# Optimization experiments

Hardware: AMD Instinct MI355X
Metric: run time of the kernel (lower is better)

The kernel has to match this reference:

```python
import jax, jax.numpy as jnp
import numpy as np

N = 20000      # nodes (B in the original code)
T = 8          # timesteps
D_IN = 256     # in_dim (must equal hid_dim due to conv_h_n reuse in original)
D_HID = 256
D_OUT = 64
E = 320000     # edges


def setup_inputs() -> dict:
    key = jax.random.key(0)
    ks = jax.random.split(key, 18)
    s = 0.05
    w = lambda k, shape: jax.random.normal(k, shape, jnp.float32) * s
    return {
        "x": jax.random.normal(ks[0], (N, T, D_IN), jnp.float32),
        "edge_index": jax.random.randint(ks[1], (2, E), 0, N),
        "W_xr": w(ks[2], (D_IN, D_HID)),  "b_xr": w(ks[3], (D_HID,)),
        "W_hr": w(ks[4], (D_HID, D_HID)), "b_hr": w(ks[5], (D_HID,)),
        "W_xz": w(ks[6], (D_IN, D_HID)),  "b_xz": w(ks[7], (D_HID,)),
        "W_hz": w(ks[8], (D_HID, D_HID)), "b_hz": w(ks[9], (D_HID,)),
        "W_hn": w(ks[10], (D_HID, D_HID)), "b_hn": w(ks[11], (D_HID,)),
        "W_fc": w(ks[12], (D_HID, D_OUT)), "b_fc": w(ks[13], (D_OUT,)),
    }


def reference(x, edge_index, W_xr, b_xr, W_hr, b_hr, W_xz, b_xz, W_hz, b_hz,
              W_hn, b_hn, W_fc, b_fc):
    n_nodes = x.shape[0]
    src, dst = edge_index[0], edge_index[1]

    # GCN symmetric normalization with self-loops (PyG GCNConv default):
    # deg[i] = 1 + #incoming edges; norm_e = d^-1/2[src]*d^-1/2[dst]
    deg = jax.ops.segment_sum(jnp.ones(src.shape[0], x.dtype), dst,
                              num_segments=n_nodes) + jnp.asarray(1.0, x.dtype)
    dis = jax.lax.rsqrt(deg)
    enorm = dis[src] * dis[dst]      # [E]
    snorm = dis * dis                # self-loop coefficient 1/deg, [N]

    def gcn(v, W, b):
        vw = v @ W                                              # [N, D]
        agg = jax.ops.segment_sum(vw[src] * enorm[:, None], dst,
                                  num_segments=n_nodes)
        return agg + vw * snorm[:, None] + b

    def step(h, x_t):
        r = jax.nn.sigmoid(gcn(x_t, W_xr, b_xr) + gcn(h, W_hr, b_hr))
        z = jax.nn.sigmoid(gcn(x_t, W_xz, b_xz) + gcn(h, W_hz, b_hz))
        # faithful to original: conv_h_n is applied to BOTH x and h
        n = jnp.tanh(gcn(x_t, W_hn, b_hn) + r * gcn(h, W_hn, b_hn))
        h_new = (1.0 - z) * h + z * n
        return h_new, None

    h0 = jnp.zeros((n_nodes, W_hr.shape[0]), x.dtype)
    h, _ = jax.lax.scan(step, h0, jnp.transpose(x, (1, 0, 2)))  # scan over T
    return h @ W_fc + b_fc
```

## Files before the change

### kernel.cpp

```cpp
#include <hip/hip_runtime.h>
#include <hip/hip_bf16.h>
#include <math.h>

#define N_NODES 20000
#define T_STEPS 8
#define DDIM    256
#define DOUT    64
#define NE      320000
#define G4      1024
#define XSTR    2048

typedef unsigned short u16;
typedef __attribute__((ext_vector_type(8))) short  short8;
typedef __attribute__((ext_vector_type(4))) float  f32x4;

__device__ __forceinline__ float bf2f(u16 u) {
    union { unsigned int i; float f; } v; v.i = ((unsigned int)u) << 16; return v.f;
}
__device__ __forceinline__ u16 f2bf(float f) {
    union { float f; unsigned int i; } v; v.f = f;
    unsigned int r = v.i + 0x7fff + ((v.i >> 16) & 1);
    return (u16)(r >> 16);
}

__global__ void k_count(const int* __restrict__ dst, int* __restrict__ cnt) {
    int e = blockIdx.x * blockDim.x + threadIdx.x;
    if (e < NE) atomicAdd(&cnt[dst[e]], 1);
}

__global__ void k_degnorm(const int* __restrict__ cnt, float* __restrict__ dis,
                          float* __restrict__ snorm) {
    int n = blockIdx.x * blockDim.x + threadIdx.x;
    if (n < N_NODES) {
        float deg = (float)(cnt[n] + 1);
        dis[n]   = rsqrtf(deg);
        snorm[n] = 1.0f / deg;
    }
}

__global__ void k_scan(const int* __restrict__ cnt, int* __restrict__ rowptr) {
    __shared__ int sums[256];
    const int CH = (N_NODES + 255) / 256;
    int t = threadIdx.x;
    int beg = t * CH;
    int end = beg + CH; if (end > N_NODES) end = N_NODES;
    int s = 0;
    for (int i = beg; i < end; i++) s += cnt[i];
    sums[t] = s;
    __syncthreads();
    if (t == 0) {
        int run = 0;
        for (int i = 0; i < 256; i++) { int v = sums[i]; sums[i] = run; run += v; }
    }
    __syncthreads();
    if (beg < N_NODES) {
        int run = sums[t];
        for (int i = beg; i < end; i++) { rowptr[i] = run; run += cnt[i]; }
        if (end == N_NODES) rowptr[N_NODES] = run;
    }
}

__global__ void k_fill(const int* __restrict__ src, const int* __restrict__ dst,
                       const int* __restrict__ rowptr, int* __restrict__ cursor,
                       const float* __restrict__ dis, int* __restrict__ csr_src,
                       float* __restrict__ csr_norm) {
    int e = blockIdx.x * blockDim.x + threadIdx.x;
    if (e < NE) {
        int d = dst[e], s = src[e];
        int pos = atomicAdd(&cursor[d], 1);
        int i = rowptr[d] + pos;
        if (i < NE) {
            csr_src[i]  = s;
            csr_norm[i] = dis[s] * dis[d];
        }
    }
}

__global__ void k_pack4T(const float* __restrict__ Wa, const float* __restrict__ Wb,
                         const float* __restrict__ Wc, const float* __restrict__ Wd,
                         u16* __restrict__ out) {
    int i = blockIdx.x * blockDim.x + threadIdx.x;
    if (i < G4 * DDIM) {
        int c = i >> 8, k = i & 255;
        const float* W = (c < 256) ? Wa : (c < 512) ? Wb : (c < 768) ? Wc : Wd;
        int cc = c & 255;
        out[i] = f2bf(W[k * DDIM + cc]);
    }
}
__global__ void k_packb4(const float* __restrict__ bxr, const float* __restrict__ bhr,
                         const float* __restrict__ bxz, const float* __restrict__ bhz,
                         const float* __restrict__ bhn, float* __restrict__ bout) {
    int c = blockIdx.x * blockDim.x + threadIdx.x;
    if (c < G4) {
        float v;
        if (c < 256)      v = bxr[c] + bhr[c];
        else if (c < 512) v = bxz[c - 256] + bhz[c - 256];
        else              v = bhn[c & 255];
        bout[c] = v;
    }
}

__global__ __launch_bounds__(256) void k_x2bf_all(const float* __restrict__ x,
                                                  u16* __restrict__ out) {
    int i = blockIdx.x * blockDim.x + threadIdx.x;
    if (i >= N_NODES * 512) return;
    size_t o = (size_t)i << 2;
    float4 v = *(const float4*)(x + o);
    ushort4 u; u.x = f2bf(v.x); u.y = f2bf(v.y); u.z = f2bf(v.z); u.w = f2bf(v.w);
    *(ushort4*)(out + o) = u;
}

__global__ __launch_bounds__(256) void k_agg_x(const u16* __restrict__ xall,
                      const int* __restrict__ rowptr, const int* __restrict__ csr_src,
                      const float* __restrict__ csr_norm, const float* __restrict__ snorm,
                      u16* __restrict__ xaall) {
    int n = blockIdx.x * 4 + (threadIdx.x >> 6);
    if (n >= N_NODES) return;
    int lane = threadIdx.x & 63;
    int c4 = lane << 2;
    float sn = snorm[n];
    float acc[8][4];
    const u16* selfp = xall + (size_t)n * XSTR + c4;
#pragma unroll
    for (int t = 0; t < 8; t++) {
        ushort4 v = *(const ushort4*)(selfp + t * DDIM);
        acc[t][0] = bf2f(v.x) * sn; acc[t][1] = bf2f(v.y) * sn;
        acc[t][2] = bf2f(v.z) * sn; acc[t][3] = bf2f(v.w) * sn;
    }
    int beg = rowptr[n], end = rowptr[n + 1];
    for (int i = beg; i < end; i++) {
        const u16* sp = xall + (size_t)csr_src[i] * XSTR + c4;
        float w = csr_norm[i];
        ushort4 g[8];
#pragma unroll
        for (int t = 0; t < 8; t++) g[t] = *(const ushort4*)(sp + t * DDIM);
#pragma unroll
        for (int t = 0; t < 8; t++) {
            acc[t][0] = fmaf(bf2f(g[t].x), w, acc[t][0]);
            acc[t][1] = fmaf(bf2f(g[t].y), w, acc[t][1]);
            acc[t][2] = fmaf(bf2f(g[t].z), w, acc[t][2]);
            acc[t][3] = fmaf(bf2f(g[t].w), w, acc[t][3]);
        }
    }
    u16* op = xaall + (size_t)n * XSTR + c4;
#pragma unroll
    for (int t = 0; t < 8; t++) {
        ushort4 o;
        o.x = f2bf(acc[t][0]); o.y = f2bf(acc[t][1]);
        o.z = f2bf(acc[t][2]); o.w = f2bf(acc[t][3]);
        *(ushort4*)(op + t * DDIM) = o;
    }
}

__global__ __launch_bounds__(256) void k_agg_bf(const u16* __restrict__ in,
                      const int* __restrict__ rowptr, const int* __restrict__ csr_src,
                      const float* __restrict__ csr_norm, const float* __restrict__ snorm,
                      u16* __restrict__ out) {
    int n = blockIdx.x * 4 + (threadIdx.x >> 6);
    if (n >= N_NODES) return;
    int lane = threadIdx.x & 63;
    int c4 = lane << 2;
    float sn = snorm[n];
    ushort4 v = *(const ushort4*)(in + (size_t)n * DDIM + c4);
    float a0 = bf2f(v.x) * sn, a1 = bf2f(v.y) * sn, a2 = bf2f(v.z) * sn, a3 = bf2f(v.w) * sn;
    int beg = rowptr[n], end = rowptr[n + 1];
    for (int i = beg; i < end; i++) {
        int s = csr_src[i];
        float w = csr_norm[i];
        ushort4 g = *(const ushort4*)(in + (size_t)s * DDIM + c4);
        a0 = fmaf(bf2f(g.x), w, a0); a1 = fmaf(bf2f(g.y), w, a1);
        a2 = fmaf(bf2f(g.z), w, a2); a3 = fmaf(bf2f(g.w), w, a3);
    }
    ushort4 o; o.x = f2bf(a0); o.y = f2bf(a1); o.z = f2bf(a2); o.w = f2bf(a3);
    *(ushort4*)(out + (size_t)n * DDIM + c4) = o;
}

__global__ __launch_bounds__(256) void k_gemm_gate(const u16* __restrict__ xa, int ldax,
        const u16* __restrict__ ha, const u16* __restrict__ BTA,
        const u16* __restrict__ BTB, const float* __restrict__ bias4,
        float* __restrict__ G, int M) {
    __shared__ u16 As[128 * 32];
    __shared__ u16 Bs[128 * 32];
    int tid  = threadIdx.x;
    int wave = tid >> 6, lane = tid & 63;
    int wr = wave >> 1, wc = wave & 1;
    int rowBase = blockIdx.x * 128;
    int cy = blockIdx.y;
    int colBase = cy * 128;
    bool use_x = (cy < 6);
    bool use_h = (cy < 4) || (cy >= 6);

    int segr  = lane >> 2;
    int chunk = (lane & 3) ^ ((segr >> 1) & 3);
    int sege  = chunk * 8;
    int ar0 = rowBase + wave * 32 + segr;
    int ar1 = ar0 + 16;
    if (ar0 > M - 1) ar0 = M - 1;
    if (ar1 > M - 1) ar1 = M - 1;
    int br0 = colBase + wave * 32 + segr;
    size_t boff0 = (size_t)br0 * DDIM + sege;
    size_t boff1 = boff0 + 16 * DDIM;
    u16* ldsA0 = &As[wave * 1024];
    u16* ldsA1 = &As[wave * 1024 + 512];
    u16* ldsB0 = &Bs[wave * 1024];
    u16* ldsB1 = &Bs[wave * 1024 + 512];

    f32x4 acc[4][4];
#pragma unroll
    for (int m = 0; m < 4; m++)
#pragma unroll
        for (int n = 0; n < 4; n++) acc[m][n] = (f32x4){0.f, 0.f, 0.f, 0.f};

    int kq  = lane >> 4;
    int lr  = lane & 15;
    int kqs = (kq ^ ((lr >> 1) & 3)) << 3;

    for (int chain = 0; chain < 2; chain++) {
        bool active = (chain == 0) ? use_x : use_h;
        if (!active) continue;
        const u16* Aop = (chain == 0) ? xa : ha;
        int lda        = (chain == 0) ? ldax : DDIM;
        const u16* BT  = (chain == 0) ? BTA : BTB;
        size_t aoff0 = (size_t)ar0 * lda + sege;
        size_t aoff1 = (size_t)ar1 * lda + sege;

        for (int k0 = 0; k0 < DDIM; k0 += 32) {
            __builtin_amdgcn_global_load_lds(
                (const __attribute__((address_space(1))) void*)(Aop + aoff0 + k0),
                (__attribute__((address_space(3))) void*)ldsA0, 16, 0, 0);
            __builtin_amdgcn_global_load_lds(
                (const __attribute__((address_space(1))) void*)(Aop + aoff1 + k0),
                (__attribute__((address_space(3))) void*)ldsA1, 16, 0, 0);
            __builtin_amdgcn_global_load_lds(
                (const __attribute__((address_space(1))) void*)(BT + boff0 + k0),
                (__attribute__((address_space(3))) void*)ldsB0, 16, 0, 0);
            __builtin_amdgcn_global_load_lds(
                (const __attribute__((address_space(1))) void*)(BT + boff1 + k0),
                (__attribute__((address_space(3))) void*)ldsB1, 16, 0, 0);
            __syncthreads();

            short8 af[4], bf[4];
#pragma unroll
            for (int m = 0; m < 4; m++)
                af[m] = *(const short8*)&As[(wr * 64 + m * 16 + lr) * 32 + kqs];
#pragma unroll
            for (int n = 0; n < 4; n++)
                bf[n] = *(const short8*)&Bs[(wc * 64 + n * 16 + lr) * 32 + kqs];
#pragma unroll
            for (int m = 0; m < 4; m++)
#pragma unroll
                for (int n = 0; n < 4; n++)
                    acc[m][n] = __builtin_amdgcn_mfma_f32_16x16x32_bf16(
                        af[m], bf[n], acc[m][n], 0, 0, 0);
            __syncthreads();
        }
    }

#pragma unroll
    for (int n = 0; n < 4; n++) {
        int col = colBase + wc * 64 + n * 16 + lr;
        float bv = bias4[col];
#pragma unroll
        for (int m = 0; m < 4; m++) {
            int row0 = rowBase + wr * 64 + m * 16 + kq * 4;
#pragma unroll
            for (int j = 0; j < 4; j++) {
                int row = row0 + j;
                if (row < M)
                    G[(size_t)row * G4 + col] = acc[m][n][j] + bv;
            }
        }
    }
}

__global__ __launch_bounds__(256) void k_gemm(const float* __restrict__ A,
        const float* __restrict__ B, const float* __restrict__ bias,
        float* __restrict__ C, int M, int N, int K) {
    __shared__ float Asm[16][132];
    __shared__ float Bsm[16][128];
    int tid = threadIdx.x;
    int tx = tid & 15, ty = tid >> 4;
    int rowBase = blockIdx.x * 128;
    int colBase = blockIdx.y * 128;

    float acc[8][8];
#pragma unroll
    for (int i = 0; i < 8; i++)
#pragma unroll
        for (int j = 0; j < 8; j++) acc[i][j] = 0.0f;

    int arow = tid >> 1;
    int acol = (tid & 1) * 8;
    int brow = tid >> 4;
    int bcol = (tid & 15) * 8;

    bool avalid = (rowBase + arow) < M;
    const float* Aptr = A + (size_t)(rowBase + arow) * K + acol;
    int bc = colBase + bcol;
    bool bvalid = bc < N;

    for (int k0 = 0; k0 < K; k0 += 16) {
        float4 a0 = {0,0,0,0}, a1 = {0,0,0,0};
        if (avalid) {
            a0 = *(const float4*)(Aptr + k0);
            a1 = *(const float4*)(Aptr + k0 + 4);
        }
        Asm[acol + 0][arow] = a0.x; Asm[acol + 1][arow] = a0.y;
        Asm[acol + 2][arow] = a0.z; Asm[acol + 3][arow] = a0.w;
        Asm[acol + 4][arow] = a1.x; Asm[acol + 5][arow] = a1.y;
        Asm[acol + 6][arow] = a1.z; Asm[acol + 7][arow] = a1.w;

        float4 b0 = {0,0,0,0}, b1 = {0,0,0,0};
        if (bvalid) {
            const float* Bp = B + (size_t)(k0 + brow) * N + bc;
            b0 = *(const float4*)(Bp);
            b1 = *(const float4*)(Bp + 4);
        }
        *(float4*)&Bsm[brow][bcol]     = b0;
        *(float4*)&Bsm[brow][bcol + 4] = b1;
        __syncthreads();

#pragma unroll
        for (int k = 0; k < 16; k++) {
            float a[8], b[8];
            *(float4*)&a[0] = *(const float4*)&Asm[k][ty * 8];
            *(float4*)&a[4] = *(const float4*)&Asm[k][ty * 8 + 4];
            *(float4*)&b[0] = *(const float4*)&Bsm[k][tx * 8];
            *(float4*)&b[4] = *(const float4*)&Bsm[k][tx * 8 + 4];
#pragma unroll
            for (int i = 0; i < 8; i++)
#pragma unroll
                for (int j = 0; j < 8; j++)
                    acc[i][j] = fmaf(a[i], b[j], acc[i][j]);
        }
        __syncthreads();
    }

    int c0 = colBase + tx * 8;
    if (c0 < N) {
        float4 bia0 = *(const float4*)(bias + c0);
        float4 bia1 = *(const float4*)(bias + c0 + 4);
#pragma unroll
        for (int i = 0; i < 8; i++) {
            int r = rowBase + ty * 8 + i;
            if (r < M) {
                float4 o0, o1;
                o0.x = acc[i][0] + bia0.x; o0.y = acc[i][1] + bia0.y;
                o0.z = acc[i][2] + bia0.z; o0.w = acc[i][3] + bia0.w;
                o1.x = acc[i][4] + bia1.x; o1.y = acc[i][5] + bia1.y;
                o1.z = acc[i][6] + bia1.z; o1.w = acc[i][7] + bia1.w;
                *(float4*)(C + (size_t)r * N + c0)     = o0;
                *(float4*)(C + (size_t)r * N + c0 + 4) = o1;
            }
        }
    }
}

__device__ __forceinline__ float sigm(float x) { return 1.0f / (1.0f + expf(-x)); }

__global__ __launch_bounds__(256) void k_gru(const float* __restrict__ G,
        float* __restrict__ h, u16* __restrict__ hbf) {
    int i = blockIdx.x * blockDim.x + threadIdx.x;
    if (i >= N_NODES * DDIM / 4) return;
    int n  = i >> 6;
    int cv = (i & 63) << 2;
    size_t gb = (size_t)n * G4 + cv;
    float4 gr  = *(const float4*)(G + gb);
    float4 gz  = *(const float4*)(G + gb + 256);
    float4 gnx = *(const float4*)(G + gb + 512);
    float4 gnh = *(const float4*)(G + gb + 768);
    float* hp = h + (size_t)n * DDIM + cv;
    float4 hv = *(float4*)hp;
    float r, z, nn;
    r = sigm(gr.x); z = sigm(gz.x);
    nn = tanhf(gnx.x + r * gnh.x); hv.x = (1.0f - z) * hv.x + z * nn;
    r = sigm(gr.y); z = sigm(gz.y);
    nn = tanhf(gnx.y + r * gnh.y); hv.y = (1.0f - z) * hv.y + z * nn;
    r = sigm(gr.z); z = sigm(gz.z);
    nn = tanhf(gnx.z + r * gnh.z); hv.z = (1.0f - z) * hv.z + z * nn;
    r = sigm(gr.w); z = sigm(gz.w);
    nn = tanhf(gnx.w + r * gnh.w); hv.w = (1.0f - z) * hv.w + z * nn;
    *(float4*)hp = hv;
    ushort4 hb; hb.x = f2bf(hv.x); hb.y = f2bf(hv.y); hb.z = f2bf(hv.z); hb.w = f2bf(hv.w);
    *(ushort4*)(hbf + (size_t)n * DDIM + cv) = hb;
}

extern "C" void kernel_launch(void* const* d_in, const int* in_sizes, int n_in,
                              void* d_out, int out_size, void* d_ws, size_t ws_size,
                              hipStream_t stream) {
    const float* x    = (const float*)d_in[0];
    const int*   eidx = (const int*)d_in[1];
    const int*   src  = eidx;
    const int*   dst  = eidx + NE;
    const float* W_xr = (const float*)d_in[2];  const float* b_xr = (const float*)d_in[3];
    const float* W_hr = (const float*)d_in[4];  const float* b_hr = (const float*)d_in[5];
    const float* W_xz = (const float*)d_in[6];  const float* b_xz = (const float*)d_in[7];
    const float* W_hz = (const float*)d_in[8];  const float* b_hz = (const float*)d_in[9];
    const float* W_hn = (const float*)d_in[10]; const float* b_hn = (const float*)d_in[11];
    const float* W_fc = (const float*)d_in[12]; const float* b_fc = (const float*)d_in[13];
    float* out = (float*)d_out;

    char* ws = (char*)d_ws;
    size_t off = 0;
    auto alloc = [&](size_t bytes) -> char* {
        char* p = ws + off;
        off += (bytes + 255) & ~(size_t)255;
        return p;
    };
    const size_t NB  = (size_t)N_NODES * DDIM * 4;
    const size_t NBH = (size_t)N_NODES * DDIM * 2;
    u16*   xall    = (u16*)alloc((size_t)N_NODES * XSTR * 2);
    u16*   xaall   = (u16*)alloc((size_t)N_NODES * XSTR * 2);
    float* G       = (float*)alloc((size_t)N_NODES * G4 * 4);
    float* h       = (float*)alloc(NB);
    u16*   hbf     = (u16*)alloc(NBH);
    u16*   ha      = (u16*)alloc(NBH);
    u16*   BTA     = (u16*)alloc((size_t)G4 * DDIM * 2);
    u16*   BTB     = (u16*)alloc((size_t)G4 * DDIM * 2);
    float* bias4   = (float*)alloc(G4 * 4);
    int*   cnt     = (int*)alloc(N_NODES * 4);
    int*   cursor  = (int*)alloc(N_NODES * 4);
    int*   rowptr  = (int*)alloc((N_NODES + 1) * 4);
    int*   csr_src = (int*)alloc(NE * 4);
    float* csr_nrm = (float*)alloc(NE * 4);
    float* dis     = (float*)alloc(N_NODES * 4);
    float* snorm   = (float*)alloc(N_NODES * 4);

    hipMemsetAsync(cnt, 0, N_NODES * 4, stream);
    hipMemsetAsync(cursor, 0, N_NODES * 4, stream);
    hipMemsetAsync(h, 0, NB, stream);
    hipMemsetAsync(hbf, 0, NBH, stream);

    const int TB = 256;
    k_count<<<(NE + TB - 1) / TB, TB, 0, stream>>>(dst, cnt);
    k_degnorm<<<(N_NODES + TB - 1) / TB, TB, 0, stream>>>(cnt, dis, snorm);
    k_scan<<<1, 256, 0, stream>>>(cnt, rowptr);
    k_fill<<<(NE + TB - 1) / TB, TB, 0, stream>>>(src, dst, rowptr, cursor, dis,
                                                  csr_src, csr_nrm);
    k_pack4T<<<(G4 * DDIM + TB - 1) / TB, TB, 0, stream>>>(W_xr, W_xz, W_hn, W_hn, BTA);
    k_pack4T<<<(G4 * DDIM + TB - 1) / TB, TB, 0, stream>>>(W_hr, W_hz, W_hn, W_hn, BTB);
    k_packb4<<<(G4 + TB - 1) / TB, TB, 0, stream>>>(b_xr, b_hr, b_xz, b_hz, b_hn, bias4);

    k_x2bf_all<<<(N_NODES * 512 + TB - 1) / TB, TB, 0, stream>>>(x, xall);
    int aggGrid = (N_NODES + 3) / 4;
    k_agg_x<<<aggGrid, TB, 0, stream>>>(xall, rowptr, csr_src, csr_nrm, snorm, xaall);

    dim3 gGate((N_NODES + 127) / 128, 8);
    dim3 gfc((N_NODES + 127) / 128, 1);
    int gruGrid = (N_NODES * DDIM / 4 + TB - 1) / TB;

    for (int t = 0; t < T_STEPS; t++) {
        k_agg_bf<<<aggGrid, TB, 0, stream>>>(hbf, rowptr, csr_src, csr_nrm, snorm, ha);
        k_gemm_gate<<<gGate, TB, 0, stream>>>(xaall + t * DDIM, XSTR, ha, BTA, BTB,
                                              bias4, G, N_NODES);
        k_gru<<<gruGrid, TB, 0, stream>>>(G, h, hbf);
    }
    k_gemm<<<gfc, TB, 0, stream>>>(h, W_fc, b_fc, out, N_NODES, DOUT, DDIM);
}
```

Before: 1.437 ms.

## Fuse gate GEMM with GRU update and unroll neighbor aggregation by two

Replaces the gate GEMM plus separate GRU elementwise kernel with one kernel. Each block computes the r, z, n-x and n-h accumulators for a 64x64 output tile from packed per-column-block weights and applies the GRU update in the epilogue. This removes the N x 1024 float gate buffer written and reread every timestep, and drops one launch per step. Both aggregation kernels now process two neighbors per iteration to raise memory-level parallelism. The cost is more accumulator registers and a smaller row tile, so the weight tile is reloaded for more row blocks.

```diff
diff --git a/kernel.cpp b/kernel.cpp
--- a/kernel.cpp
+++ b/kernel.cpp
@@ -7,7 +7,6 @@
 #define DDIM    256
 #define DOUT    64
 #define NE      320000
-#define G4      1024
 #define XSTR    2048
 
 typedef unsigned short u16;
@@ -76,26 +75,31 @@
     }
 }
 
-__global__ void k_pack4T(const float* __restrict__ Wa, const float* __restrict__ Wb,
-                         const float* __restrict__ Wc, const float* __restrict__ Wd,
-                         u16* __restrict__ out) {
+__global__ void k_pack6(const float* __restrict__ Wxr, const float* __restrict__ Wxz,
+                        const float* __restrict__ Whn, const float* __restrict__ Whr,
+                        const float* __restrict__ Whz, u16* __restrict__ out) {
     int i = blockIdx.x * blockDim.x + threadIdx.x;
-    if (i < G4 * DDIM) {
-        int c = i >> 8, k = i & 255;
-        const float* W = (c < 256) ? Wa : (c < 512) ? Wb : (c < 768) ? Wc : Wd;
-        int cc = c & 255;
-        out[i] = f2bf(W[k * DDIM + cc]);
-    }
-}
-__global__ void k_packb4(const float* __restrict__ bxr, const float* __restrict__ bhr,
+    if (i >= 4 * 6 * 64 * 256) return;
+    int k    = i & 255;
+    int c    = (i >> 8) & 63;
+    int tile = (i >> 14) % 6;
+    int by   = i / (6 * 64 * 256);
+    const float* W;
+    switch (tile) {
+        case 0: W = Wxr; break; case 1: W = Wxz; break; case 2: W = Whn; break;
+        case 3: W = Whr; break; case 4: W = Whz; break; default: W = Whn; break;
+    }
+    out[i] = f2bf(W[k * DDIM + by * 64 + c]);
+}
+__global__ void k_packb3(const float* __restrict__ bxr, const float* __restrict__ bhr,
                          const float* __restrict__ bxz, const float* __restrict__ bhz,
                          const float* __restrict__ bhn, float* __restrict__ bout) {
     int c = blockIdx.x * blockDim.x + threadIdx.x;
-    if (c < G4) {
+    if (c < 3 * DDIM) {
         float v;
         if (c < 256)      v = bxr[c] + bhr[c];
         else if (c < 512) v = bxz[c - 256] + bhz[c - 256];
-        else              v = bhn[c & 255];
+        else              v = bhn[c - 512];
         bout[c] = v;
     }
 }
@@ -128,18 +132,34 @@
         acc[t][2] = bf2f(v.z) * sn; acc[t][3] = bf2f(v.w) * sn;
     }
     int beg = rowptr[n], end = rowptr[n + 1];
-    for (int i = beg; i < end; i++) {
+    int i = beg;
+    for (; i + 1 < end; i += 2) {
+        const u16* sp0 = xall + (size_t)csr_src[i] * XSTR + c4;
+        const u16* sp1 = xall + (size_t)csr_src[i + 1] * XSTR + c4;
+        float w0 = csr_norm[i], w1 = csr_norm[i + 1];
+        ushort4 g0[8], g1[8];
+#pragma unroll
+        for (int t = 0; t < 8; t++) g0[t] = *(const ushort4*)(sp0 + t * DDIM);
+#pragma unroll
+        for (int t = 0; t < 8; t++) g1[t] = *(const ushort4*)(sp1 + t * DDIM);
+#pragma unroll
+        for (int t = 0; t < 8; t++) {
+            acc[t][0] = fmaf(bf2f(g0[t].x), w0, fmaf(bf2f(g1[t].x), w1, acc[t][0]));
+            acc[t][1] = fmaf(bf2f(g0[t].y), w0, fmaf(bf2f(g1[t].y), w1, acc[t][1]));
+            acc[t][2] = fmaf(bf2f(g0[t].z), w0, fmaf(bf2f(g1[t].z), w1, acc[t][2]));
+            acc[t][3] = fmaf(bf2f(g0[t].w), w0, fmaf(bf2f(g1[t].w), w1, acc[t][3]));
+        }
+    }
+    if (i < end) {
         const u16* sp = xall + (size_t)csr_src[i] * XSTR + c4;
         float w = csr_norm[i];
-        ushort4 g[8];
-#pragma unroll
-        for (int t = 0; t < 8; t++) g[t] = *(const ushort4*)(sp + t * DDIM);
 #pragma unroll
         for (int t = 0; t < 8; t++) {
-            acc[t][0] = fmaf(bf2f(g[t].x), w, acc[t][0]);
-            acc[t][1] = fmaf(bf2f(g[t].y), w, acc[t][1]);
-            acc[t][2] = fmaf(bf2f(g[t].z), w, acc[t][2]);
-            acc[t][3] = fmaf(bf2f(g[t].w), w, acc[t][3]);
+            ushort4 g = *(const ushort4*)(sp + t * DDIM);
+            acc[t][0] = fmaf(bf2f(g.x), w, acc[t][0]);
+            acc[t][1] = fmaf(bf2f(g.y), w, acc[t][1]);
+            acc[t][2] = fmaf(bf2f(g.z), w, acc[t][2]);
+            acc[t][3] = fmaf(bf2f(g.w), w, acc[t][3]);
         }
     }
     u16* op = xaall + (size_t)n * XSTR + c4;
@@ -164,10 +184,19 @@
     ushort4 v = *(const ushort4*)(in + (size_t)n * DDIM + c4);
     float a0 = bf2f(v.x) * sn, a1 = bf2f(v.y) * sn, a2 = bf2f(v.z) * sn, a3 = bf2f(v.w) * sn;
     int beg = rowptr[n], end = rowptr[n + 1];
-    for (int i = beg; i < end; i++) {
-        int s = csr_src[i];
+    int i = beg;
+    for (; i + 1 < end; i += 2) {
+        ushort4 g0 = *(const ushort4*)(in + (size_t)csr_src[i] * DDIM + c4);
+        ushort4 g1 = *(const ushort4*)(in + (size_t)csr_src[i + 1] * DDIM + c4);
+        float w0 = csr_norm[i], w1 = csr_norm[i + 1];
+        a0 = fmaf(bf2f(g0.x), w0, fmaf(bf2f(g1.x), w1, a0));
+        a1 = fmaf(bf2f(g0.y), w0, fmaf(bf2f(g1.y), w1, a1));
+        a2 = fmaf(bf2f(g0.z), w0, fmaf(bf2f(g1.z), w1, a2));
+        a3 = fmaf(bf2f(g0.w), w0, fmaf(bf2f(g1.w), w1, a3));
+    }
+    if (i < end) {
+        ushort4 g = *(const ushort4*)(in + (size_t)csr_src[i] * DDIM + c4);
         float w = csr_norm[i];
-        ushort4 g = *(const ushort4*)(in + (size_t)s * DDIM + c4);
         a0 = fmaf(bf2f(g.x), w, a0); a1 = fmaf(bf2f(g.y), w, a1);
         a2 = fmaf(bf2f(g.z), w, a2); a3 = fmaf(bf2f(g.w), w, a3);
     }
@@ -175,99 +204,110 @@
     *(ushort4*)(out + (size_t)n * DDIM + c4) = o;
 }
 
-__global__ __launch_bounds__(256) void k_gemm_gate(const u16* __restrict__ xa, int ldax,
-        const u16* __restrict__ ha, const u16* __restrict__ BTA,
-        const u16* __restrict__ BTB, const float* __restrict__ bias4,
-        float* __restrict__ G, int M) {
-    __shared__ u16 As[128 * 32];
-    __shared__ u16 Bs[128 * 32];
-    int tid  = threadIdx.x;
-    int wave = tid >> 6, lane = tid & 63;
-    int wr = wave >> 1, wc = wave & 1;
-    int rowBase = blockIdx.x * 128;
-    int cy = blockIdx.y;
-    int colBase = cy * 128;
-    bool use_x = (cy < 6);
-    bool use_h = (cy < 4) || (cy >= 6);
-
-    int segr  = lane >> 2;
-    int chunk = (lane & 3) ^ ((segr >> 1) & 3);
+__device__ __forceinline__ float sigm(float x) { return 1.0f / (1.0f + expf(-x)); }
+
+__global__ __launch_bounds__(256) void k_gate_gru(const u16* __restrict__ xa, int ldax,
+        const u16* __restrict__ ha, const u16* __restrict__ BTpack,
+        const float* __restrict__ bias3, float* __restrict__ h, u16* __restrict__ hbf,
+        int M) {
+    __shared__ u16 Axs[64 * 32];
+    __shared__ u16 Ahs[64 * 32];
+    __shared__ u16 Bs[6 * 64 * 32];
+    int tid = threadIdx.x;
+    int w = tid >> 6, lane = tid & 63;
+    int rowBase = blockIdx.x * 64;
+    int by = blockIdx.y;
+
+    int srow  = lane >> 2;
+    int chunk = (lane & 3) ^ ((lane >> 3) & 3);
     int sege  = chunk * 8;
-    int ar0 = rowBase + wave * 32 + segr;
-    int ar1 = ar0 + 16;
-    if (ar0 > M - 1) ar0 = M - 1;
-    if (ar1 > M - 1) ar1 = M - 1;
-    int br0 = colBase + wave * 32 + segr;
-    size_t boff0 = (size_t)br0 * DDIM + sege;
-    size_t boff1 = boff0 + 16 * DDIM;
-    u16* ldsA0 = &As[wave * 1024];
-    u16* ldsA1 = &As[wave * 1024 + 512];
-    u16* ldsB0 = &Bs[wave * 1024];
-    u16* ldsB1 = &Bs[wave * 1024 + 512];
-
-    f32x4 acc[4][4];
-#pragma unroll
-    for (int m = 0; m < 4; m++)
-#pragma unroll
-        for (int n = 0; n < 4; n++) acc[m][n] = (f32x4){0.f, 0.f, 0.f, 0.f};
-
-    int kq  = lane >> 4;
-    int lr  = lane & 15;
+    int arow = rowBase + w * 16 + srow;
+    if (arow > M - 1) arow = M - 1;
+    size_t xoff = (size_t)arow * ldax + sege;
+    size_t hoff = (size_t)arow * DDIM + sege;
+    u16* ldsAx = &Axs[w * 16 * 32];
+    u16* ldsAh = &Ahs[w * 16 * 32];
+    const u16* Bbase = BTpack + (size_t)by * (6 * 64 * 256);
+
+    f32x4 ar[2][2], az[2][2], anx[2][2], anh[2][2];
+#pragma unroll
+    for (int m = 0; m < 2; m++)
+#pragma unroll
+        for (int n = 0; n < 2; n++) {
+            ar[m][n] = (f32x4){0.f,0.f,0.f,0.f}; az[m][n] = (f32x4){0.f,0.f,0.f,0.f};
+            anx[m][n] = (f32x4){0.f,0.f,0.f,0.f}; anh[m][n] = (f32x4){0.f,0.f,0.f,0.f};
+        }
+
+    int kq = lane >> 4, lr = lane & 15;
     int kqs = (kq ^ ((lr >> 1) & 3)) << 3;
 
-    for (int chain = 0; chain < 2; chain++) {
-        bool active = (chain == 0) ? use_x : use_h;
-        if (!active) continue;
-        const u16* Aop = (chain == 0) ? xa : ha;
-        int lda        = (chain == 0) ? ldax : DDIM;
-        const u16* BT  = (chain == 0) ? BTA : BTB;
-        size_t aoff0 = (size_t)ar0 * lda + sege;
-        size_t aoff1 = (size_t)ar1 * lda + sege;
-
-        for (int k0 = 0; k0 < DDIM; k0 += 32) {
+    for (int k0 = 0; k0 < DDIM; k0 += 32) {
+        __builtin_amdgcn_global_load_lds(
+            (const __attribute__((address_space(1))) void*)(xa + xoff + k0),
+            (__attribute__((address_space(3))) void*)ldsAx, 16, 0, 0);
+        __builtin_amdgcn_global_load_lds(
+            (const __attribute__((address_space(1))) void*)(ha + hoff + k0),
+            (__attribute__((address_space(3))) void*)ldsAh, 16, 0, 0);
+#pragma unroll
+        for (int j6 = 0; j6 < 6; j6++) {
+            int j = w * 6 + j6;
+            int tile = j >> 2, q = j & 3;
+            const u16* src = Bbase + ((size_t)tile * 64 + q * 16 + srow) * 256 + k0 + sege;
+            u16* dst = &Bs[tile * 2048 + q * 512];
             __builtin_amdgcn_global_load_lds(
-                (const __attribute__((address_space(1))) void*)(Aop + aoff0 + k0),
-                (__attribute__((address_space(3))) void*)ldsA0, 16, 0, 0);
-            __builtin_amdgcn_global_load_lds(
-                (const __attribute__((address_space(1))) void*)(Aop + aoff1 + k0),
-                (__attribute__((address_space(3))) void*)ldsA1, 16, 0, 0);
-            __builtin_amdgcn_global_load_lds(
-                (const __attribute__((address_space(1))) void*)(BT + boff0 + k0),
-                (__attribute__((address_space(3))) void*)ldsB0, 16, 0, 0);
-            __builtin_amdgcn_global_load_lds(
-                (const __attribute__((address_space(1))) void*)(BT + boff1 + k0),
-                (__attribute__((address_space(3))) void*)ldsB1, 16, 0, 0);
-            __syncthreads();
-
-            short8 af[4], bf[4];
-#pragma unroll
-            for (int m = 0; m < 4; m++)
-                af[m] = *(const short8*)&As[(wr * 64 + m * 16 + lr) * 32 + kqs];
-#pragma unroll
-            for (int n = 0; n < 4; n++)
-                bf[n] = *(const short8*)&Bs[(wc * 64 + n * 16 + lr) * 32 + kqs];
-#pragma unroll
-            for (int m = 0; m < 4; m++)
-#pragma unroll
-                for (int n = 0; n < 4; n++)
-                    acc[m][n] = __builtin_amdgcn_mfma_f32_16x16x32_bf16(
-                        af[m], bf[n], acc[m][n], 0, 0, 0);
-            __syncthreads();
-        }
-    }
-
-#pragma unroll
-    for (int n = 0; n < 4; n++) {
-        int col = colBase + wc * 64 + n * 16 + lr;
-        float bv = bias4[col];
-#pragma unroll
-        for (int m = 0; m < 4; m++) {
-            int row0 = rowBase + wr * 64 + m * 16 + kq * 4;
+                (const __attribute__((address_space(1))) void*)src,
+                (__attribute__((address_space(3))) void*)dst, 16, 0, 0);
+        }
+        __syncthreads();
+
+        short8 ax[2], ah[2], bf[6][2];
+#pragma unroll
+        for (int m = 0; m < 2; m++) {
+            int r = (w >> 1) * 32 + m * 16 + lr;
+            ax[m] = *(const short8*)&Axs[r * 32 + kqs];
+            ah[m] = *(const short8*)&Ahs[r * 32 + kqs];
+        }
+#pragma unroll
+        for (int t = 0; t < 6; t++)
+#pragma unroll
+            for (int n = 0; n < 2; n++) {
+                int c = (w & 1) * 32 + n * 16 + lr;
+                bf[t][n] = *(const short8*)&Bs[t * 2048 + c * 32 + kqs];
+            }
+#pragma unroll
+        for (int m = 0; m < 2; m++)
+#pragma unroll
+            for (int n = 0; n < 2; n++) {
+                ar[m][n]  = __builtin_amdgcn_mfma_f32_16x16x32_bf16(ax[m], bf[0][n], ar[m][n], 0, 0, 0);
+                ar[m][n]  = __builtin_amdgcn_mfma_f32_16x16x32_bf16(ah[m], bf[3][n], ar[m][n], 0, 0, 0);
+                az[m][n]  = __builtin_amdgcn_mfma_f32_16x16x32_bf16(ax[m], bf[1][n], az[m][n], 0, 0, 0);
+                az[m][n]  = __builtin_amdgcn_mfma_f32_16x16x32_bf16(ah[m], bf[4][n], az[m][n], 0, 0, 0);
+                anx[m][n] = __builtin_amdgcn_mfma_f32_16x16x32_bf16(ax[m], bf[2][n], anx[m][n], 0, 0, 0);
+                anh[m][n] = __builtin_amdgcn_mfma_f32_16x16x32_bf16(ah[m], bf[5][n], anh[m][n], 0, 0, 0);
+            }
+        __syncthreads();
+    }
+
+#pragma unroll
+    for (int n = 0; n < 2; n++) {
+        int col = by * 64 + (w & 1) * 32 + n * 16 + lr;
+        float br = bias3[col], bz = bias3[256 + col], bn = bias3[512 + col];
+#pragma unroll
+        for (int m = 0; m < 2; m++) {
+            int row0 = rowBase + (w >> 1) * 32 + m * 16 + kq * 4;
 #pragma unroll
             for (int j = 0; j < 4; j++) {
                 int row = row0 + j;
-                if (row < M)
-                    G[(size_t)row * G4 + col] = acc[m][n][j] + bv;
+                if (row < M) {
+                    float r = sigm(ar[m][n][j] + br);
+                    float z = sigm(az[m][n][j] + bz);
+                    float nn = tanhf(anx[m][n][j] + bn + r * (anh[m][n][j] + bn));
+                    size_t idx = (size_t)row * DDIM + col;
+                    float hv = h[idx];
+                    hv = (1.0f - z) * hv + z * nn;
+                    h[idx] = hv;
+                    hbf[idx] = f2bf(hv);
+                }
             }
         }
     }
@@ -354,35 +394,6 @@
             }
         }
     }
-}
-
-__device__ __forceinline__ float sigm(float x) { return 1.0f / (1.0f + expf(-x)); }
-
-__global__ __launch_bounds__(256) void k_gru(const float* __restrict__ G,
-        float* __restrict__ h, u16* __restrict__ hbf) {
-    int i = blockIdx.x * blockDim.x + threadIdx.x;
-    if (i >= N_NODES * DDIM / 4) return;
-    int n  = i >> 6;
-    int cv = (i & 63) << 2;
-    size_t gb = (size_t)n * G4 + cv;
-    float4 gr  = *(const float4*)(G + gb);
-    float4 gz  = *(const float4*)(G + gb + 256);
-    float4 gnx = *(const float4*)(G + gb + 512);
-    float4 gnh = *(const float4*)(G + gb + 768);
-    float* hp = h + (size_t)n * DDIM + cv;
-    float4 hv = *(float4*)hp;
-    float r, z, nn;
-    r = sigm(gr.x); z = sigm(gz.x);
-    nn = tanhf(gnx.x + r * gnh.x); hv.x = (1.0f - z) * hv.x + z * nn;
-    r = sigm(gr.y); z = sigm(gz.y);
-    nn = tanhf(gnx.y + r * gnh.y); hv.y = (1.0f - z) * hv.y + z * nn;
-    r = sigm(gr.z); z = sigm(gz.z);
-    nn = tanhf(gnx.z + r * gnh.z); hv.z = (1.0f - z) * hv.z + z * nn;
-    r = sigm(gr.w); z = sigm(gz.w);
-    nn = tanhf(gnx.w + r * gnh.w); hv.w = (1.0f - z) * hv.w + z * nn;
-    *(float4*)hp = hv;
-    ushort4 hb; hb.x = f2bf(hv.x); hb.y = f2bf(hv.y); hb.z = f2bf(hv.z); hb.w = f2bf(hv.w);
-    *(ushort4*)(hbf + (size_t)n * DDIM + cv) = hb;
 }
 
 extern "C" void kernel_launch(void* const* d_in, const int* in_sizes, int n_in,
@@ -411,13 +422,11 @@
     const size_t NBH = (size_t)N_NODES * DDIM * 2;
     u16*   xall    = (u16*)alloc((size_t)N_NODES * XSTR * 2);
     u16*   xaall   = (u16*)alloc((size_t)N_NODES * XSTR * 2);
-    float* G       = (float*)alloc((size_t)N_NODES * G4 * 4);
     float* h       = (float*)alloc(NB);
     u16*   hbf     = (u16*)alloc(NBH);
     u16*   ha      = (u16*)alloc(NBH);
-    u16*   BTA     = (u16*)alloc((size_t)G4 * DDIM * 2);
-    u16*   BTB     = (u16*)alloc((size_t)G4 * DDIM * 2);
-    float* bias4   = (float*)alloc(G4 * 4);
+    u16*   BTpack  = (u16*)alloc((size_t)4 * 6 * 64 * 256 * 2);
+    float* bias3   = (float*)alloc(3 * DDIM * 4);
     int*   cnt     = (int*)alloc(N_NODES * 4);
     int*   cursor  = (int*)alloc(N_NODES * 4);
     int*   rowptr  = (int*)alloc((N_NODES + 1) * 4);
@@ -437,23 +446,22 @@
     k_scan<<<1, 256, 0, stream>>>(cnt, rowptr);
     k_fill<<<(NE + TB - 1) / TB, TB, 0, stream>>>(src, dst, rowptr, cursor, dis,
                                                   csr_src, csr_nrm);
-    k_pack4T<<<(G4 * DDIM + TB - 1) / TB, TB, 0, stream>>>(W_xr, W_xz, W_hn, W_hn, BTA);
-    k_pack4T<<<(G4 * DDIM + TB - 1) / TB, TB, 0, stream>>>(W_hr, W_hz, W_hn, W_hn, BTB);
-    k_packb4<<<(G4 + TB - 1) / TB, TB, 0, stream>>>(b_xr, b_hr, b_xz, b_hz, b_hn, bias4);
+    k_pack6<<<(4 * 6 * 64 * 256 + TB - 1) / TB, TB, 0, stream>>>(W_xr, W_xz, W_hn,
+                                                                 W_hr, W_hz, BTpack);
+    k_packb3<<<(3 * DDIM + TB - 1) / TB, TB, 0, stream>>>(b_xr, b_hr, b_xz, b_hz,
+                                                          b_hn, bias3);
 
     k_x2bf_all<<<(N_NODES * 512 + TB - 1) / TB, TB, 0, stream>>>(x, xall);
     int aggGrid = (N_NODES + 3) / 4;
     k_agg_x<<<aggGrid, TB, 0, stream>>>(xall, rowptr, csr_src, csr_nrm, snorm, xaall);
 
-    dim3 gGate((N_NODES + 127) / 128, 8);
+    dim3 gGate((N_NODES + 63) / 64, 4);
     dim3 gfc((N_NODES + 127) / 128, 1);
-    int gruGrid = (N_NODES * DDIM / 4 + TB - 1) / TB;
 
     for (int t = 0; t < T_STEPS; t++) {
         k_agg_bf<<<aggGrid, TB, 0, stream>>>(hbf, rowptr, csr_src, csr_nrm, snorm, ha);
-        k_gemm_gate<<<gGate, TB, 0, stream>>>(xaall + t * DDIM, XSTR, ha, BTA, BTB,
-                                              bias4, G, N_NODES);
-        k_gru<<<gruGrid, TB, 0, stream>>>(G, h, hbf);
+        k_gate_gru<<<gGate, TB, 0, stream>>>(xaall + t * DDIM, XSTR, ha, BTpack,
+                                             bias3, h, hbf, N_NODES);
     }
     k_gemm<<<gfc, TB, 0, stream>>>(h, W_fc, b_fc, out, N_NODES, DOUT, DDIM);
 }
```

Result: faster. 1.216 ms (-15.4%).
